# Kernel optimization log

Measured on AMD Instinct MI355X. Metric: run time of the kernel, lower is better.

Reference implementation:

```python
import math
import jax, jax.numpy as jnp
import numpy as np

B, T, C = 1, 2048, 4096
N_HEAD, N_KV_HEAD = 32, 8
HEAD_DIM = C // N_HEAD          # 128
N_REP = N_HEAD // N_KV_HEAD     # 4
HIDDEN = 11008                  # SwiGLU hidden: multiple_of=256 rounding of 2/3*4*C
EPS = 1e-6
ROPE_THETA = 10000.0


def _rms_norm(x, w, eps=EPS):
    # x: [B,T,C] float32; matches RMSNorm._norm in fp32
    inv = jax.lax.rsqrt(jnp.mean(x * x, axis=-1, keepdims=True) + eps)
    return (x * inv) * w


def _apply_rope(t, cos, sin):
    # t: [B,T,H,D]; cos/sin: [T,D/2]; interleaved complex rotation as in apply_rotary_emb
    tr = t.reshape(*t.shape[:-1], HEAD_DIM // 2, 2)
    re, im = tr[..., 0], tr[..., 1]
    c = cos[None, :, None, :]
    s = sin[None, :, None, :]
    out_re = re * c - im * s
    out_im = re * s + im * c
    return jnp.stack([out_re, out_im], axis=-1).reshape(t.shape)


def setup_inputs() -> dict:
    key = jax.random.key(0)
    ks = jax.random.split(key, 10)
    x = jax.random.normal(ks[0], (B, T, C), dtype=jnp.float32)
    # RoPE frequencies (theta=10000)
    inv_freq = 1.0 / (ROPE_THETA ** (np.arange(0, HEAD_DIM, 2, dtype=np.float32) / HEAD_DIM))
    angles = np.outer(np.arange(T, dtype=np.float32), inv_freq)  # [T, D/2]
    freqs_cos = jnp.asarray(np.cos(angles), dtype=jnp.float32)
    freqs_sin = jnp.asarray(np.sin(angles), dtype=jnp.float32)
    # causal additive mask [T,T]
    mask = jnp.triu(jnp.full((T, T), -1e9, dtype=jnp.float32), k=1)
    sc = 0.02
    wq = jax.random.normal(ks[1], (N_HEAD * HEAD_DIM, C), dtype=jnp.float32) * sc
    wk = jax.random.normal(ks[2], (N_KV_HEAD * HEAD_DIM, C), dtype=jnp.float32) * sc
    wv = jax.random.normal(ks[3], (N_KV_HEAD * HEAD_DIM, C), dtype=jnp.float32) * sc
    wo = jax.random.normal(ks[4], (C, N_HEAD * HEAD_DIM), dtype=jnp.float32) * sc
    w1 = jax.random.normal(ks[5], (HIDDEN, C), dtype=jnp.float32) * sc
    w2 = jax.random.normal(ks[6], (C, HIDDEN), dtype=jnp.float32) * sc
    w3 = jax.random.normal(ks[7], (HIDDEN, C), dtype=jnp.float32) * sc
    ln1_w = jnp.ones((C,), dtype=jnp.float32)
    ln2_w = jnp.ones((C,), dtype=jnp.float32)
    return {"x": x, "start_pos": 0, "freqs_cos": freqs_cos, "freqs_sin": freqs_sin,
            "mask": mask, "wq": wq, "wk": wk, "wv": wv, "wo": wo,
            "w1": w1, "w2": w2, "w3": w3, "ln1_w": ln1_w, "ln2_w": ln2_w}


def reference(x, start_pos, freqs_cos, freqs_sin, mask, wq, wk, wv, wo, w1, w2, w3, ln1_w, ln2_w):
    # --- attention branch (pre-norm) ---
    xn = _rms_norm(x, ln1_w)
    q = (xn @ wq.T).reshape(B, T, N_HEAD, HEAD_DIM)
    k = (xn @ wk.T).reshape(B, T, N_KV_HEAD, HEAD_DIM)
    v = (xn @ wv.T).reshape(B, T, N_KV_HEAD, HEAD_DIM)
    q = _apply_rope(q, freqs_cos, freqs_sin)
    k = _apply_rope(k, freqs_cos, freqs_sin)
    # prefill (start_pos==0): cache slice [:start_pos+T] == current k/v
    keys = jnp.repeat(k, N_REP, axis=2)    # GQA repeat_kv -> [B,T,32,128]
    values = jnp.repeat(v, N_REP, axis=2)
    scores = jnp.einsum('bqhd,bkhd->bhqk', q, keys) / math.sqrt(HEAD_DIM)
    scores = scores + mask[None, None, :, :]
    probs = jax.nn.softmax(scores.astype(jnp.float32), axis=-1)
    attn = jnp.einsum('bhqk,bkhd->bqhd', probs, values).reshape(B, T, C)
    x = x + attn @ wo.T
    # --- SwiGLU FFN branch (pre-norm) ---
    xn2 = _rms_norm(x, ln2_w)
    h = jax.nn.silu(xn2 @ w1.T) * (xn2 @ w3.T)
    x = x + h @ w2.T
    return x
```

## Files before the change

kernel.cpp:

```cpp
#include <hip/hip_runtime.h>
#include <stdint.h>

#define T_SEQ 2048
#define C_DIM 4096
#define NHEAD 32
#define NKV 8
#define HD 128
#define HIDDEN 11008

typedef float f32x4 __attribute__((ext_vector_type(4)));
typedef __bf16 bf16x8 __attribute__((ext_vector_type(8)));
typedef __attribute__((address_space(1))) const void* gptr_t;
typedef __attribute__((address_space(3))) void* lptr_t;

__device__ __forceinline__ unsigned short f2bf(float f) {
  unsigned u = __float_as_uint(f);
  u += 0x7fffu + ((u >> 16) & 1u);
  return (unsigned short)(u >> 16);
}
__device__ __forceinline__ float bf2f(unsigned short h) {
  return __uint_as_float(((unsigned)h) << 16);
}

template <typename OutT, bool RESID>
__global__ __launch_bounds__(256) void gemm_bt(
    const unsigned short* A, int lda, long sAz,
    const unsigned short* B, int ldb, long sBz, int bzShift,
    OutT* C, int ldc, long sCz,
    const float* R,
    int M, int N, int K)
{
  const int z = blockIdx.z;
  A += (long)z * sAz;
  B += (long)(z >> bzShift) * sBz;
  C += (long)z * sCz;
  const float* Rz = R + (long)z * sCz;

  __shared__ unsigned short lA[128 * 64];
  __shared__ unsigned short lB[128 * 64];

  const int t    = threadIdx.x;
  const int lane = t & 63;
  const int srow = t >> 3;
  const int scolL = (t & 7) << 3;
  const int scolG = (((t & 7) ^ (srow & 7)) << 3);
  const int wave = t >> 6;
  const int wr   = (wave >> 1) << 6;
  const int wc   = (wave & 1) << 6;
  const int m16  = lane & 15;
  const int quad = lane >> 4;
  const int rl   = lane & 7;

  const long tileM = (long)blockIdx.y * 128;
  const long tileN = (long)blockIdx.x * 128;

  f32x4 acc[4][4] = {};

  const unsigned short* Abase = A + (tileM + srow) * lda + scolG;
  const unsigned short* Bbase = B + (tileN + srow) * ldb + scolG;

  for (int k0 = 0; k0 < K; k0 += 64) {
#pragma unroll
    for (int s = 0; s < 4; ++s) {
      const unsigned short* ga = Abase + (long)(s * 32) * lda + k0;
      const unsigned short* gb = Bbase + (long)(s * 32) * ldb + k0;
      unsigned short* la = &lA[(s * 32 + srow) * 64 + scolL];
      unsigned short* lb = &lB[(s * 32 + srow) * 64 + scolL];
      __builtin_amdgcn_global_load_lds((gptr_t)ga, (lptr_t)la, 16, 0, 0);
      __builtin_amdgcn_global_load_lds((gptr_t)gb, (lptr_t)lb, 16, 0, 0);
    }
    __syncthreads();
#pragma unroll
    for (int kk = 0; kk < 64; kk += 32) {
      const int ca = ((((kk >> 4) >> 1) + quad) ^ rl) << 3;
      bf16x8 af[4], bfr[4];
#pragma unroll
      for (int i = 0; i < 4; ++i)
        af[i] = *(const bf16x8*)&lA[(wr + i * 16 + m16) * 64 + ((((kk >> 3) + quad) ^ rl) << 3)];
#pragma unroll
      for (int j = 0; j < 4; ++j)
        bfr[j] = *(const bf16x8*)&lB[(wc + j * 16 + m16) * 64 + ((((kk >> 3) + quad) ^ rl) << 3)];
      (void)ca;
#pragma unroll
      for (int i = 0; i < 4; ++i)
#pragma unroll
        for (int j = 0; j < 4; ++j)
          acc[i][j] = __builtin_amdgcn_mfma_f32_16x16x32_bf16(af[i], bfr[j], acc[i][j], 0, 0, 0);
    }
    __syncthreads();
  }

#pragma unroll
  for (int i = 0; i < 4; ++i) {
#pragma unroll
    for (int j = 0; j < 4; ++j) {
      const long row = tileM + wr + i * 16 + quad * 4;
      const long col = tileN + wc + j * 16 + m16;
#pragma unroll
      for (int r = 0; r < 4; ++r) {
        const long off = (row + r) * (long)ldc + col;
        float v = acc[i][j][r];
        if constexpr (RESID) v += Rz[off];
        if constexpr (sizeof(OutT) == 2) C[off] = f2bf(v);
        else                             C[off] = v;
      }
    }
  }
}

__global__ __launch_bounds__(256) void rmsnorm_kernel(
    const float* __restrict__ x, const float* __restrict__ w,
    unsigned short* __restrict__ out)
{
  const int row = blockIdx.x;
  const int t = threadIdx.x;
  const float4* xr = (const float4*)(x + (long)row * C_DIM);
  float4 xv[4];
  float s = 0.f;
#pragma unroll
  for (int i = 0; i < 4; ++i) {
    float4 a = xr[t * 4 + i];
    xv[i] = a;
    s += a.x * a.x + a.y * a.y + a.z * a.z + a.w * a.w;
  }
#pragma unroll
  for (int off = 32; off > 0; off >>= 1) s += __shfl_down(s, off);
  __shared__ float red[4];
  if ((t & 63) == 0) red[t >> 6] = s;
  __syncthreads();
  const float inv = rsqrtf((red[0] + red[1] + red[2] + red[3]) * (1.f / C_DIM) + 1e-6f);
  const float4* wr4 = (const float4*)w;
  ushort4* o = (ushort4*)(out + (long)row * C_DIM);
#pragma unroll
  for (int i = 0; i < 4; ++i) {
    float4 a = xv[i];
    float4 ww = wr4[t * 4 + i];
    ushort4 r;
    r.x = f2bf(a.x * inv * ww.x); r.y = f2bf(a.y * inv * ww.y);
    r.z = f2bf(a.z * inv * ww.z); r.w = f2bf(a.w * inv * ww.w);
    o[t * 4 + i] = r;
  }
}

__global__ __launch_bounds__(256) void cvt_kernel(
    const float* __restrict__ in, unsigned short* __restrict__ out)
{
  const long i = (long)blockIdx.x * 256 + threadIdx.x;
  float4 f = ((const float4*)in)[i];
  ushort4 r;
  r.x = f2bf(f.x); r.y = f2bf(f.y); r.z = f2bf(f.z); r.w = f2bf(f.w);
  ((ushort4*)out)[i] = r;
}

template <int NHd>
__global__ __launch_bounds__(256) void rope_kernel(
    unsigned short* tq, const float* __restrict__ cp, const float* __restrict__ sp)
{
  constexpr int SH = (NHd == 32) ? 5 : 3;
  const long idx = (long)blockIdx.x * 256 + threadIdx.x;
  const int i = (int)(idx & 63);
  const long rest = idx >> 6;
  const int h = (int)(rest & (NHd - 1));
  const int t = (int)(rest >> SH);
  const long base = (((long)t * NHd + h) << 7) + 2 * i;
  const float re = bf2f(tq[base]);
  const float im = bf2f(tq[base + 1]);
  const float c = cp[t * 64 + i];
  const float s = sp[t * 64 + i];
  tq[base]     = f2bf(re * c - im * s);
  tq[base + 1] = f2bf(re * s + im * c);
}

__global__ __launch_bounds__(256) void transpose_v(
    const unsigned short* __restrict__ v, unsigned short* __restrict__ vt)
{
  const long idx = (long)blockIdx.x * 256 + threadIdx.x;
  const int t = (int)(idx & 2047);
  const int kvd = (int)(idx >> 11);
  vt[idx] = v[(long)t * 1024 + kvd];
}

__global__ __launch_bounds__(256) void softmax_kernel(float* scores)
{
  const int q = blockIdx.x;
  const long z = blockIdx.y;
  float* row = scores + (z * T_SEQ + q) * (long)T_SEQ;
  unsigned short* orow = (unsigned short*)(scores + z * (long)T_SEQ * T_SEQ) + (long)q * 2 * T_SEQ;
  const int t = threadIdx.x;
  const int base = t * 8;
  float4 a = ((const float4*)row)[t * 2];
  float4 b = ((const float4*)row)[t * 2 + 1];
  float v[8] = {a.x, a.y, a.z, a.w, b.x, b.y, b.z, b.w};
  const float scale = 0.08838834764831845f;
  float mx = -INFINITY;
#pragma unroll
  for (int j = 0; j < 8; ++j) {
    v[j] = (base + j <= q) ? v[j] * scale : -INFINITY;
    mx = fmaxf(mx, v[j]);
  }
#pragma unroll
  for (int off = 32; off > 0; off >>= 1) mx = fmaxf(mx, __shfl_down(mx, off));
  __shared__ float redm[4], reds[4];
  if ((t & 63) == 0) redm[t >> 6] = mx;
  __syncthreads();
  mx = fmaxf(fmaxf(redm[0], redm[1]), fmaxf(redm[2], redm[3]));
  float s = 0.f;
#pragma unroll
  for (int j = 0; j < 8; ++j) {
    float e = (base + j <= q) ? __expf(v[j] - mx) : 0.f;
    v[j] = e;
    s += e;
  }
#pragma unroll
  for (int off = 32; off > 0; off >>= 1) s += __shfl_down(s, off);
  if ((t & 63) == 0) reds[t >> 6] = s;
  __syncthreads();
  s = reds[0] + reds[1] + reds[2] + reds[3];
  const float inv = 1.f / s;
  ushort4 o0, o1;
  o0.x = f2bf(v[0] * inv); o0.y = f2bf(v[1] * inv);
  o0.z = f2bf(v[2] * inv); o0.w = f2bf(v[3] * inv);
  o1.x = f2bf(v[4] * inv); o1.y = f2bf(v[5] * inv);
  o1.z = f2bf(v[6] * inv); o1.w = f2bf(v[7] * inv);
  ((ushort4*)orow)[t * 2]     = o0;
  ((ushort4*)orow)[t * 2 + 1] = o1;
}

__global__ __launch_bounds__(256) void silu_mul_kernel(
    const unsigned short* __restrict__ g1, const unsigned short* __restrict__ g3,
    unsigned short* __restrict__ h)
{
  const long i = (long)blockIdx.x * 256 + threadIdx.x;
  ushort4 a4 = ((const ushort4*)g1)[i];
  ushort4 b4 = ((const ushort4*)g3)[i];
  ushort4 r;
  { float a = bf2f(a4.x), b = bf2f(b4.x); r.x = f2bf(a / (1.f + __expf(-a)) * b); }
  { float a = bf2f(a4.y), b = bf2f(b4.y); r.y = f2bf(a / (1.f + __expf(-a)) * b); }
  { float a = bf2f(a4.z), b = bf2f(b4.z); r.z = f2bf(a / (1.f + __expf(-a)) * b); }
  { float a = bf2f(a4.w), b = bf2f(b4.w); r.w = f2bf(a / (1.f + __expf(-a)) * b); }
  ((ushort4*)h)[i] = r;
}

extern "C" void kernel_launch(void* const* d_in, const int* in_sizes, int n_in,
                              void* d_out, int out_size, void* d_ws, size_t ws_size,
                              hipStream_t stream) {
  const float* x    = (const float*)d_in[0];
  const float* fcos = (const float*)d_in[2];
  const float* fsin = (const float*)d_in[3];
  const float* wq   = (const float*)d_in[5];
  const float* wk   = (const float*)d_in[6];
  const float* wv   = (const float*)d_in[7];
  const float* wo   = (const float*)d_in[8];
  const float* w1   = (const float*)d_in[9];
  const float* w2   = (const float*)d_in[10];
  const float* w3   = (const float*)d_in[11];
  const float* ln1  = (const float*)d_in[12];
  const float* ln2  = (const float*)d_in[13];
  float* out = (float*)d_out;

  char* p = (char*)d_ws;
  auto alloc = [&](size_t bytes) { char* r = p; p += (bytes + 255) & ~(size_t)255; return r; };
  unsigned short* Wb   = (unsigned short*)alloc((size_t)HIDDEN * C_DIM * 2);
  unsigned short* xn   = (unsigned short*)alloc((size_t)T_SEQ * C_DIM * 2);
  unsigned short* qb   = (unsigned short*)alloc((size_t)T_SEQ * C_DIM * 2);
  unsigned short* kb   = (unsigned short*)alloc((size_t)T_SEQ * 1024 * 2);
  unsigned short* vb   = (unsigned short*)alloc((size_t)T_SEQ * 1024 * 2);
  unsigned short* vt   = (unsigned short*)alloc((size_t)T_SEQ * 1024 * 2);
  unsigned short* attn = (unsigned short*)alloc((size_t)T_SEQ * C_DIM * 2);
  const size_t scoresB = (size_t)8 * T_SEQ * T_SEQ * 4;
  const size_t ffnB    = (size_t)T_SEQ * C_DIM * 2 + 3ULL * T_SEQ * HIDDEN * 2;
  char* regC = alloc(scoresB > ffnB ? scoresB : ffnB);
  float* scores = (float*)regC;
  unsigned short* xn2 = (unsigned short*)regC;
  unsigned short* g1  = (unsigned short*)(regC + (size_t)T_SEQ * C_DIM * 2);
  unsigned short* g3  = (unsigned short*)(regC + (size_t)T_SEQ * C_DIM * 2 + (size_t)T_SEQ * HIDDEN * 2);
  unsigned short* hb  = (unsigned short*)(regC + (size_t)T_SEQ * C_DIM * 2 + 2ULL * T_SEQ * HIDDEN * 2);

  rmsnorm_kernel<<<T_SEQ, 256, 0, stream>>>(x, ln1, xn);

  cvt_kernel<<<(C_DIM * C_DIM) / 1024, 256, 0, stream>>>(wq, Wb);
  gemm_bt<unsigned short, false><<<dim3(C_DIM / 128, T_SEQ / 128, 1), 256, 0, stream>>>(
      xn, C_DIM, 0, Wb, C_DIM, 0, 0, qb, C_DIM, 0, nullptr, T_SEQ, C_DIM, C_DIM);
  cvt_kernel<<<(1024 * C_DIM) / 1024, 256, 0, stream>>>(wk, Wb);
  gemm_bt<unsigned short, false><<<dim3(1024 / 128, T_SEQ / 128, 1), 256, 0, stream>>>(
      xn, C_DIM, 0, Wb, C_DIM, 0, 0, kb, 1024, 0, nullptr, T_SEQ, 1024, C_DIM);
  cvt_kernel<<<(1024 * C_DIM) / 1024, 256, 0, stream>>>(wv, Wb);
  gemm_bt<unsigned short, false><<<dim3(1024 / 128, T_SEQ / 128, 1), 256, 0, stream>>>(
      xn, C_DIM, 0, Wb, C_DIM, 0, 0, vb, 1024, 0, nullptr, T_SEQ, 1024, C_DIM);

  rope_kernel<NHEAD><<<(T_SEQ * NHEAD * 64) / 256, 256, 0, stream>>>(qb, fcos, fsin);
  rope_kernel<NKV><<<(T_SEQ * NKV * 64) / 256, 256, 0, stream>>>(kb, fcos, fsin);
  transpose_v<<<(T_SEQ * 1024) / 256, 256, 0, stream>>>(vb, vt);

  for (int c = 0; c < 4; ++c) {
    gemm_bt<float, false><<<dim3(T_SEQ / 128, T_SEQ / 128, 8), 256, 0, stream>>>(
        qb + c * 1024, C_DIM, 128,
        kb + c * 256, 1024, 128, 2,
        scores, T_SEQ, (long)T_SEQ * T_SEQ, nullptr,
        T_SEQ, T_SEQ, HD);
    softmax_kernel<<<dim3(T_SEQ, 8), 256, 0, stream>>>(scores);
    gemm_bt<unsigned short, false><<<dim3(1, T_SEQ / 128, 8), 256, 0, stream>>>(
        (unsigned short*)scores, 2 * T_SEQ, (long)T_SEQ * 2 * T_SEQ,
        vt + (size_t)c * 2 * HD * T_SEQ, T_SEQ, (long)HD * T_SEQ, 2,
        attn + c * 1024, C_DIM, 128, nullptr,
        T_SEQ, HD, T_SEQ);
  }

  cvt_kernel<<<(C_DIM * C_DIM) / 1024, 256, 0, stream>>>(wo, Wb);
  gemm_bt<float, true><<<dim3(C_DIM / 128, T_SEQ / 128, 1), 256, 0, stream>>>(
      attn, C_DIM, 0, Wb, C_DIM, 0, 0, out, C_DIM, 0, x, T_SEQ, C_DIM, C_DIM);

  rmsnorm_kernel<<<T_SEQ, 256, 0, stream>>>(out, ln2, xn2);
  cvt_kernel<<<((size_t)HIDDEN * C_DIM) / 1024, 256, 0, stream>>>(w1, Wb);
  gemm_bt<unsigned short, false><<<dim3(HIDDEN / 128, T_SEQ / 128, 1), 256, 0, stream>>>(
      xn2, C_DIM, 0, Wb, C_DIM, 0, 0, g1, HIDDEN, 0, nullptr, T_SEQ, HIDDEN, C_DIM);
  cvt_kernel<<<((size_t)HIDDEN * C_DIM) / 1024, 256, 0, stream>>>(w3, Wb);
  gemm_bt<unsigned short, false><<<dim3(HIDDEN / 128, T_SEQ / 128, 1), 256, 0, stream>>>(
      xn2, C_DIM, 0, Wb, C_DIM, 0, 0, g3, HIDDEN, 0, nullptr, T_SEQ, HIDDEN, C_DIM);
  silu_mul_kernel<<<((size_t)T_SEQ * HIDDEN) / 1024, 256, 0, stream>>>(g1, g3, hb);
  cvt_kernel<<<((size_t)C_DIM * HIDDEN) / 1024, 256, 0, stream>>>(w2, Wb);
  gemm_bt<float, true><<<dim3(C_DIM / 128, T_SEQ / 128, 1), 256, 0, stream>>>(
      hb, HIDDEN, 0, Wb, HIDDEN, 0, 0, out, C_DIM, 0, out, T_SEQ, C_DIM, HIDDEN);
}
```

Measured before the change: 2.138 ms.

## Fuse QKV GEMM, store bf16 scores, batch all heads, templatize GEMM strides

New measurement: 1.788 ms. 16.4% less time.

```diff
diff --git a/kernel.cpp b/kernel.cpp
--- a/kernel.cpp
+++ b/kernel.cpp
@@ -7,6 +7,7 @@
 #define NKV 8
 #define HD 128
 #define HIDDEN 11008
+#define QKV_W (C_DIM + 2 * NKV * HD)
 
 typedef float f32x4 __attribute__((ext_vector_type(4)));
 typedef __bf16 bf16x8 __attribute__((ext_vector_type(8)));
@@ -22,65 +23,76 @@
   return __uint_as_float(((unsigned)h) << 16);
 }
 
-template <typename OutT, bool RESID>
+template <typename OutT, bool RESID, int LDA, int LDB, int LDC, int K,
+          long SAZ, long SBZ, int BZSH, long SCZ>
 __global__ __launch_bounds__(256) void gemm_bt(
-    const unsigned short* A, int lda, long sAz,
-    const unsigned short* B, int ldb, long sBz, int bzShift,
-    OutT* C, int ldc, long sCz,
-    const float* R,
-    int M, int N, int K)
+    const unsigned short* __restrict__ A, const unsigned short* __restrict__ B,
+    OutT* __restrict__ C, const float* __restrict__ R)
 {
   const int z = blockIdx.z;
-  A += (long)z * sAz;
-  B += (long)(z >> bzShift) * sBz;
-  C += (long)z * sCz;
-  const float* Rz = R + (long)z * sCz;
+  A += (long)z * SAZ;
+  B += (long)(z >> BZSH) * SBZ;
+  C += (long)z * SCZ;
+  const float* Rz = RESID ? (R + (long)z * SCZ) : nullptr;
 
   __shared__ unsigned short lA[128 * 64];
   __shared__ unsigned short lB[128 * 64];
 
-  const int t    = threadIdx.x;
-  const int lane = t & 63;
-  const int srow = t >> 3;
+  const int t     = threadIdx.x;
+  const int lane  = t & 63;
+  const int srow  = t >> 3;
   const int scolL = (t & 7) << 3;
   const int scolG = (((t & 7) ^ (srow & 7)) << 3);
-  const int wave = t >> 6;
-  const int wr   = (wave >> 1) << 6;
-  const int wc   = (wave & 1) << 6;
-  const int m16  = lane & 15;
-  const int quad = lane >> 4;
-  const int rl   = lane & 7;
+  const int wave  = t >> 6;
+  const int wr    = (wave >> 1) << 6;
+  const int wc    = (wave & 1) << 6;
+  const int m16   = lane & 15;
+  const int quad  = lane >> 4;
+  const int rl    = lane & 7;
+  const int c0    = ((quad ^ rl) << 3);
+  const int c1    = (((4 + quad) ^ rl) << 3);
 
   const long tileM = (long)blockIdx.y * 128;
   const long tileN = (long)blockIdx.x * 128;
 
   f32x4 acc[4][4] = {};
 
-  const unsigned short* Abase = A + (tileM + srow) * lda + scolG;
-  const unsigned short* Bbase = B + (tileN + srow) * ldb + scolG;
+  const unsigned short* Aptr = A + (tileM + srow) * LDA + scolG;
+  const unsigned short* Bptr = B + (tileN + srow) * LDB + scolG;
 
   for (int k0 = 0; k0 < K; k0 += 64) {
 #pragma unroll
     for (int s = 0; s < 4; ++s) {
-      const unsigned short* ga = Abase + (long)(s * 32) * lda + k0;
-      const unsigned short* gb = Bbase + (long)(s * 32) * ldb + k0;
-      unsigned short* la = &lA[(s * 32 + srow) * 64 + scolL];
-      unsigned short* lb = &lB[(s * 32 + srow) * 64 + scolL];
-      __builtin_amdgcn_global_load_lds((gptr_t)ga, (lptr_t)la, 16, 0, 0);
-      __builtin_amdgcn_global_load_lds((gptr_t)gb, (lptr_t)lb, 16, 0, 0);
-    }
+      __builtin_amdgcn_global_load_lds((gptr_t)(Aptr + s * 32 * LDA),
+                                       (lptr_t)&lA[(s * 32 + srow) * 64 + scolL], 16, 0, 0);
+      __builtin_amdgcn_global_load_lds((gptr_t)(Bptr + s * 32 * LDB),
+                                       (lptr_t)&lB[(s * 32 + srow) * 64 + scolL], 16, 0, 0);
+    }
+    Aptr += 64;
+    Bptr += 64;
     __syncthreads();
-#pragma unroll
-    for (int kk = 0; kk < 64; kk += 32) {
-      const int ca = ((((kk >> 4) >> 1) + quad) ^ rl) << 3;
+    {
       bf16x8 af[4], bfr[4];
 #pragma unroll
       for (int i = 0; i < 4; ++i)
-        af[i] = *(const bf16x8*)&lA[(wr + i * 16 + m16) * 64 + ((((kk >> 3) + quad) ^ rl) << 3)];
+        af[i] = *(const bf16x8*)&lA[(wr + i * 16 + m16) * 64 + c0];
 #pragma unroll
       for (int j = 0; j < 4; ++j)
-        bfr[j] = *(const bf16x8*)&lB[(wc + j * 16 + m16) * 64 + ((((kk >> 3) + quad) ^ rl) << 3)];
-      (void)ca;
+        bfr[j] = *(const bf16x8*)&lB[(wc + j * 16 + m16) * 64 + c0];
+#pragma unroll
+      for (int i = 0; i < 4; ++i)
+#pragma unroll
+        for (int j = 0; j < 4; ++j)
+          acc[i][j] = __builtin_amdgcn_mfma_f32_16x16x32_bf16(af[i], bfr[j], acc[i][j], 0, 0, 0);
+    }
+    {
+      bf16x8 af[4], bfr[4];
+#pragma unroll
+      for (int i = 0; i < 4; ++i)
+        af[i] = *(const bf16x8*)&lA[(wr + i * 16 + m16) * 64 + c1];
+#pragma unroll
+      for (int j = 0; j < 4; ++j)
+        bfr[j] = *(const bf16x8*)&lB[(wc + j * 16 + m16) * 64 + c1];
 #pragma unroll
       for (int i = 0; i < 4; ++i)
 #pragma unroll
@@ -98,7 +110,7 @@
       const long col = tileN + wc + j * 16 + m16;
 #pragma unroll
       for (int r = 0; r < 4; ++r) {
-        const long off = (row + r) * (long)ldc + col;
+        const long off = (row + r) * (long)LDC + col;
         float v = acc[i][j][r];
         if constexpr (RESID) v += Rz[off];
         if constexpr (sizeof(OutT) == 2) C[off] = f2bf(v);
@@ -152,7 +164,7 @@
   ((ushort4*)out)[i] = r;
 }
 
-template <int NHd>
+template <int NHd, int COFF>
 __global__ __launch_bounds__(256) void rope_kernel(
     unsigned short* tq, const float* __restrict__ cp, const float* __restrict__ sp)
 {
@@ -162,7 +174,7 @@
   const long rest = idx >> 6;
   const int h = (int)(rest & (NHd - 1));
   const int t = (int)(rest >> SH);
-  const long base = (((long)t * NHd + h) << 7) + 2 * i;
+  const long base = (long)t * QKV_W + COFF + h * HD + 2 * i;
   const float re = bf2f(tq[base]);
   const float im = bf2f(tq[base + 1]);
   const float c = cp[t * 64 + i];
@@ -172,25 +184,25 @@
 }
 
 __global__ __launch_bounds__(256) void transpose_v(
-    const unsigned short* __restrict__ v, unsigned short* __restrict__ vt)
+    const unsigned short* __restrict__ qkvb, unsigned short* __restrict__ vt)
 {
   const long idx = (long)blockIdx.x * 256 + threadIdx.x;
   const int t = (int)(idx & 2047);
   const int kvd = (int)(idx >> 11);
-  vt[idx] = v[(long)t * 1024 + kvd];
-}
-
-__global__ __launch_bounds__(256) void softmax_kernel(float* scores)
+  vt[idx] = qkvb[(long)t * QKV_W + (C_DIM + NKV * HD) + kvd];
+}
+
+__global__ __launch_bounds__(256) void softmax_bf16(unsigned short* scores)
 {
   const int q = blockIdx.x;
   const long z = blockIdx.y;
-  float* row = scores + (z * T_SEQ + q) * (long)T_SEQ;
-  unsigned short* orow = (unsigned short*)(scores + z * (long)T_SEQ * T_SEQ) + (long)q * 2 * T_SEQ;
+  unsigned short* row = scores + (z * T_SEQ + q) * (long)T_SEQ;
   const int t = threadIdx.x;
   const int base = t * 8;
-  float4 a = ((const float4*)row)[t * 2];
-  float4 b = ((const float4*)row)[t * 2 + 1];
-  float v[8] = {a.x, a.y, a.z, a.w, b.x, b.y, b.z, b.w};
+  ushort4 a4 = ((const ushort4*)row)[t * 2];
+  ushort4 b4 = ((const ushort4*)row)[t * 2 + 1];
+  float v[8] = {bf2f(a4.x), bf2f(a4.y), bf2f(a4.z), bf2f(a4.w),
+                bf2f(b4.x), bf2f(b4.y), bf2f(b4.z), bf2f(b4.w)};
   const float scale = 0.08838834764831845f;
   float mx = -INFINITY;
 #pragma unroll
@@ -222,8 +234,8 @@
   o0.z = f2bf(v[2] * inv); o0.w = f2bf(v[3] * inv);
   o1.x = f2bf(v[4] * inv); o1.y = f2bf(v[5] * inv);
   o1.z = f2bf(v[6] * inv); o1.w = f2bf(v[7] * inv);
-  ((ushort4*)orow)[t * 2]     = o0;
-  ((ushort4*)orow)[t * 2 + 1] = o1;
+  ((ushort4*)row)[t * 2]     = o0;
+  ((ushort4*)row)[t * 2 + 1] = o1;
 }
 
 __global__ __launch_bounds__(256) void silu_mul_kernel(
@@ -262,63 +274,69 @@
   auto alloc = [&](size_t bytes) { char* r = p; p += (bytes + 255) & ~(size_t)255; return r; };
   unsigned short* Wb   = (unsigned short*)alloc((size_t)HIDDEN * C_DIM * 2);
   unsigned short* xn   = (unsigned short*)alloc((size_t)T_SEQ * C_DIM * 2);
-  unsigned short* qb   = (unsigned short*)alloc((size_t)T_SEQ * C_DIM * 2);
-  unsigned short* kb   = (unsigned short*)alloc((size_t)T_SEQ * 1024 * 2);
-  unsigned short* vb   = (unsigned short*)alloc((size_t)T_SEQ * 1024 * 2);
+  unsigned short* qkvb = (unsigned short*)alloc((size_t)T_SEQ * QKV_W * 2);
   unsigned short* vt   = (unsigned short*)alloc((size_t)T_SEQ * 1024 * 2);
   unsigned short* attn = (unsigned short*)alloc((size_t)T_SEQ * C_DIM * 2);
-  const size_t scoresB = (size_t)8 * T_SEQ * T_SEQ * 4;
-  const size_t ffnB    = (size_t)T_SEQ * C_DIM * 2 + 3ULL * T_SEQ * HIDDEN * 2;
-  char* regC = alloc(scoresB > ffnB ? scoresB : ffnB);
-  float* scores = (float*)regC;
+  const size_t scoresAllB = (size_t)NHEAD * T_SEQ * T_SEQ * 2;
+  const size_t scoresChkB = (size_t)8 * T_SEQ * T_SEQ * 2;
+  const size_t ffnB = (size_t)T_SEQ * C_DIM * 2 + 3ULL * T_SEQ * HIDDEN * 2;
+  const size_t usedSoFar = (size_t)(p - (char*)d_ws);
+  const bool allHeads = ws_size >= usedSoFar + (scoresAllB > ffnB ? scoresAllB : ffnB) + 1024;
+  char* regC = alloc((allHeads ? scoresAllB : (scoresChkB > ffnB ? scoresChkB : ffnB)) > ffnB
+                         ? (allHeads ? scoresAllB : (scoresChkB > ffnB ? scoresChkB : ffnB))
+                         : ffnB);
+  unsigned short* scores = (unsigned short*)regC;
   unsigned short* xn2 = (unsigned short*)regC;
   unsigned short* g1  = (unsigned short*)(regC + (size_t)T_SEQ * C_DIM * 2);
   unsigned short* g3  = (unsigned short*)(regC + (size_t)T_SEQ * C_DIM * 2 + (size_t)T_SEQ * HIDDEN * 2);
   unsigned short* hb  = (unsigned short*)(regC + (size_t)T_SEQ * C_DIM * 2 + 2ULL * T_SEQ * HIDDEN * 2);
 
+  constexpr long TT = (long)T_SEQ * T_SEQ;
+
   rmsnorm_kernel<<<T_SEQ, 256, 0, stream>>>(x, ln1, xn);
 
   cvt_kernel<<<(C_DIM * C_DIM) / 1024, 256, 0, stream>>>(wq, Wb);
-  gemm_bt<unsigned short, false><<<dim3(C_DIM / 128, T_SEQ / 128, 1), 256, 0, stream>>>(
-      xn, C_DIM, 0, Wb, C_DIM, 0, 0, qb, C_DIM, 0, nullptr, T_SEQ, C_DIM, C_DIM);
-  cvt_kernel<<<(1024 * C_DIM) / 1024, 256, 0, stream>>>(wk, Wb);
-  gemm_bt<unsigned short, false><<<dim3(1024 / 128, T_SEQ / 128, 1), 256, 0, stream>>>(
-      xn, C_DIM, 0, Wb, C_DIM, 0, 0, kb, 1024, 0, nullptr, T_SEQ, 1024, C_DIM);
-  cvt_kernel<<<(1024 * C_DIM) / 1024, 256, 0, stream>>>(wv, Wb);
-  gemm_bt<unsigned short, false><<<dim3(1024 / 128, T_SEQ / 128, 1), 256, 0, stream>>>(
-      xn, C_DIM, 0, Wb, C_DIM, 0, 0, vb, 1024, 0, nullptr, T_SEQ, 1024, C_DIM);
-
-  rope_kernel<NHEAD><<<(T_SEQ * NHEAD * 64) / 256, 256, 0, stream>>>(qb, fcos, fsin);
-  rope_kernel<NKV><<<(T_SEQ * NKV * 64) / 256, 256, 0, stream>>>(kb, fcos, fsin);
-  transpose_v<<<(T_SEQ * 1024) / 256, 256, 0, stream>>>(vb, vt);
-
-  for (int c = 0; c < 4; ++c) {
-    gemm_bt<float, false><<<dim3(T_SEQ / 128, T_SEQ / 128, 8), 256, 0, stream>>>(
-        qb + c * 1024, C_DIM, 128,
-        kb + c * 256, 1024, 128, 2,
-        scores, T_SEQ, (long)T_SEQ * T_SEQ, nullptr,
-        T_SEQ, T_SEQ, HD);
-    softmax_kernel<<<dim3(T_SEQ, 8), 256, 0, stream>>>(scores);
-    gemm_bt<unsigned short, false><<<dim3(1, T_SEQ / 128, 8), 256, 0, stream>>>(
-        (unsigned short*)scores, 2 * T_SEQ, (long)T_SEQ * 2 * T_SEQ,
-        vt + (size_t)c * 2 * HD * T_SEQ, T_SEQ, (long)HD * T_SEQ, 2,
-        attn + c * 1024, C_DIM, 128, nullptr,
-        T_SEQ, HD, T_SEQ);
+  cvt_kernel<<<(NKV * HD * C_DIM) / 1024, 256, 0, stream>>>(wk, Wb + (size_t)C_DIM * C_DIM);
+  cvt_kernel<<<(NKV * HD * C_DIM) / 1024, 256, 0, stream>>>(wv, Wb + (size_t)(C_DIM + NKV * HD) * C_DIM);
+  gemm_bt<unsigned short, false, C_DIM, C_DIM, QKV_W, C_DIM, 0, 0, 0, 0>
+      <<<dim3(QKV_W / 128, T_SEQ / 128, 1), 256, 0, stream>>>(xn, Wb, qkvb, nullptr);
+
+  rope_kernel<NHEAD, 0><<<(T_SEQ * NHEAD * 64) / 256, 256, 0, stream>>>(qkvb, fcos, fsin);
+  rope_kernel<NKV, C_DIM><<<(T_SEQ * NKV * 64) / 256, 256, 0, stream>>>(qkvb, fcos, fsin);
+  transpose_v<<<(T_SEQ * 1024) / 256, 256, 0, stream>>>(qkvb, vt);
+
+  if (allHeads) {
+    gemm_bt<unsigned short, false, QKV_W, QKV_W, T_SEQ, HD, HD, HD, 2, TT>
+        <<<dim3(T_SEQ / 128, T_SEQ / 128, NHEAD), 256, 0, stream>>>(
+            qkvb, qkvb + C_DIM, scores, nullptr);
+    softmax_bf16<<<dim3(T_SEQ, NHEAD), 256, 0, stream>>>(scores);
+    gemm_bt<unsigned short, false, T_SEQ, T_SEQ, C_DIM, T_SEQ, TT, (long)HD * T_SEQ, 2, HD>
+        <<<dim3(1, T_SEQ / 128, NHEAD), 256, 0, stream>>>(scores, vt, attn, nullptr);
+  } else {
+    for (int c = 0; c < 4; ++c) {
+      gemm_bt<unsigned short, false, QKV_W, QKV_W, T_SEQ, HD, HD, HD, 2, TT>
+          <<<dim3(T_SEQ / 128, T_SEQ / 128, 8), 256, 0, stream>>>(
+              qkvb + c * 1024, qkvb + C_DIM + c * 256, scores, nullptr);
+      softmax_bf16<<<dim3(T_SEQ, 8), 256, 0, stream>>>(scores);
+      gemm_bt<unsigned short, false, T_SEQ, T_SEQ, C_DIM, T_SEQ, TT, (long)HD * T_SEQ, 2, HD>
+          <<<dim3(1, T_SEQ / 128, 8), 256, 0, stream>>>(
+              scores, vt + (size_t)c * 256 * T_SEQ, attn + c * 1024, nullptr);
+    }
   }
 
   cvt_kernel<<<(C_DIM * C_DIM) / 1024, 256, 0, stream>>>(wo, Wb);
-  gemm_bt<float, true><<<dim3(C_DIM / 128, T_SEQ / 128, 1), 256, 0, stream>>>(
-      attn, C_DIM, 0, Wb, C_DIM, 0, 0, out, C_DIM, 0, x, T_SEQ, C_DIM, C_DIM);
+  gemm_bt<float, true, C_DIM, C_DIM, C_DIM, C_DIM, 0, 0, 0, 0>
+      <<<dim3(C_DIM / 128, T_SEQ / 128, 1), 256, 0, stream>>>(attn, Wb, out, x);
 
   rmsnorm_kernel<<<T_SEQ, 256, 0, stream>>>(out, ln2, xn2);
   cvt_kernel<<<((size_t)HIDDEN * C_DIM) / 1024, 256, 0, stream>>>(w1, Wb);
-  gemm_bt<unsigned short, false><<<dim3(HIDDEN / 128, T_SEQ / 128, 1), 256, 0, stream>>>(
-      xn2, C_DIM, 0, Wb, C_DIM, 0, 0, g1, HIDDEN, 0, nullptr, T_SEQ, HIDDEN, C_DIM);
+  gemm_bt<unsigned short, false, C_DIM, C_DIM, HIDDEN, C_DIM, 0, 0, 0, 0>
+      <<<dim3(HIDDEN / 128, T_SEQ / 128, 1), 256, 0, stream>>>(xn2, Wb, g1, nullptr);
   cvt_kernel<<<((size_t)HIDDEN * C_DIM) / 1024, 256, 0, stream>>>(w3, Wb);
-  gemm_bt<unsigned short, false><<<dim3(HIDDEN / 128, T_SEQ / 128, 1), 256, 0, stream>>>(
-      xn2, C_DIM, 0, Wb, C_DIM, 0, 0, g3, HIDDEN, 0, nullptr, T_SEQ, HIDDEN, C_DIM);
+  gemm_bt<unsigned short, false, C_DIM, C_DIM, HIDDEN, C_DIM, 0, 0, 0, 0>
+      <<<dim3(HIDDEN / 128, T_SEQ / 128, 1), 256, 0, stream>>>(xn2, Wb, g3, nullptr);
   silu_mul_kernel<<<((size_t)T_SEQ * HIDDEN) / 1024, 256, 0, stream>>>(g1, g3, hb);
   cvt_kernel<<<((size_t)C_DIM * HIDDEN) / 1024, 256, 0, stream>>>(w2, Wb);
-  gemm_bt<float, true><<<dim3(C_DIM / 128, T_SEQ / 128, 1), 256, 0, stream>>>(
-      hb, HIDDEN, 0, Wb, HIDDEN, 0, 0, out, C_DIM, 0, out, T_SEQ, C_DIM, HIDDEN);
-}
+  gemm_bt<float, true, HIDDEN, HIDDEN, C_DIM, HIDDEN, 0, 0, 0, 0>
+      <<<dim3(C_DIM / 128, T_SEQ / 128, 1), 256, 0, stream>>>(hb, Wb, out, out);
+}
```
